# Kernel tuning notes

Hardware: AMD Instinct MI355X
Metric: run time of the kernel (lower is better)

## Reference

```python
import jax, jax.numpy as jnp
import numpy as np

NEG_SLOPE = 0.01  # torch nn.LeakyReLU default

N_NODES = 100000
N_EDGES = 1000000
D_FEAT = 64


def setup_inputs() -> dict:
    key = jax.random.key(0)
    ks = jax.random.split(key, 8)
    x = jax.random.normal(ks[0], (N_NODES, D_FEAT), dtype=jnp.float32)
    src = jax.random.randint(ks[1], (N_EDGES,), 0, N_NODES, dtype=jnp.int64 if jax.config.jax_enable_x64 else jnp.int32)
    dst = jax.random.randint(ks[2], (N_EDGES,), 0, N_NODES, dtype=jnp.int64 if jax.config.jax_enable_x64 else jnp.int32)
    s = 1.0 / np.sqrt(D_FEAT)
    W1 = jax.random.normal(ks[3], (D_FEAT, 64), dtype=jnp.float32) * s
    b1 = jnp.zeros((64,), dtype=jnp.float32)
    W2 = jax.random.normal(ks[4], (64, 64), dtype=jnp.float32) * s
    b2 = jnp.zeros((64,), dtype=jnp.float32)
    Wc = jax.random.normal(ks[5], (64, 2), dtype=jnp.float32) * s
    bc = jnp.zeros((2,), dtype=jnp.float32)
    return {"x": x, "src": src, "dst": dst, "W1": W1, "b1": b1,
            "W2": W2, "b2": b2, "Wc": Wc, "bc": bc}


def _graph_conv(x, src, dst, W, b, out_deg_isqrt, in_deg_isqrt, n_nodes):
    # DGL GraphConv, norm='both': h_v = ( sum_{u->v} x_u / sqrt(d_out(u)) ) / sqrt(d_in(v)) @ W + b
    # (in_feats <= out_feats here, so aggregate first then transform, matching DGL order)
    h = x * out_deg_isqrt[:, None]          # [N, d] scale by source out-degree
    msg = h[src]                            # [E, d] gather
    agg = jax.ops.segment_sum(msg, dst, num_segments=n_nodes)  # [N, d] scatter-add
    agg = agg * in_deg_isqrt[:, None]
    return agg @ W + b


def reference(x, src, dst, W1, b1, W2, b2, Wc, bc):
    n = x.shape[0]
    ones_e = jnp.ones(src.shape[0], dtype=x.dtype)
    out_deg = jnp.clip(jax.ops.segment_sum(ones_e, src, num_segments=n), 1.0)
    in_deg = jnp.clip(jax.ops.segment_sum(ones_e, dst, num_segments=n), 1.0)
    out_isqrt = out_deg ** -0.5
    in_isqrt = in_deg ** -0.5

    h = _graph_conv(x, src, dst, W1, b1, out_isqrt, in_isqrt, n)
    h = jax.nn.leaky_relu(h, NEG_SLOPE)
    h = _graph_conv(h, src, dst, W2, b2, out_isqrt, in_isqrt, n)
    h = jax.nn.leaky_relu(h, NEG_SLOPE)
    return h @ Wc + bc  # prediction=True -> linear classifier
```

## Files before the change

### kernel.cpp

```cpp
#include <hip/hip_runtime.h>


typedef __attribute__((ext_vector_type(8))) short short8;
typedef __attribute__((ext_vector_type(4))) float f32x4;

#define NPB 256
#define BSH 9
#define BW  512

__device__ __forceinline__ float b2f(unsigned short u) {
    return __uint_as_float(((unsigned int)u) << 16);
}
__device__ __forceinline__ unsigned short f2b(float f) {
    unsigned int i = __float_as_uint(f);
    unsigned int r = (i + 0x7FFFu + ((i >> 16) & 1u)) >> 16;
    return (unsigned short)r;
}

__global__ __launch_bounds__(256) void count_kernel(
    const int* __restrict__ src, const int* __restrict__ dst,
    int* __restrict__ cntD, int* __restrict__ cntS, int e, int chunk) {
    __shared__ int hD[256], hS[256];
    int t = threadIdx.x, pb = blockIdx.x;
    hD[t] = 0; hS[t] = 0;
    __syncthreads();
    int e0 = pb * chunk, e1 = min(e, e0 + chunk);
    for (int i = e0 + t; i < e1; i += 256) {
        atomicAdd(&hD[dst[i] >> BSH], 1);
        atomicAdd(&hS[src[i] >> BSH], 1);
    }
    __syncthreads();
    cntD[t * NPB + pb] = hD[t];
    cntS[t * NPB + pb] = hS[t];
}

__global__ __launch_bounds__(1024) void scanmat_kernel(int* __restrict__ cntD,
                                                       int* __restrict__ cntS) {
    int* a = (blockIdx.x == 0) ? cntD : cntS;
    __shared__ int s[1024];
    int t = threadIdx.x;
    int base = t * 64;
    int sum = 0;
    for (int j = 0; j < 64; j++) sum += a[base + j];
    s[t] = sum;
    __syncthreads();
    for (int d = 1; d < 1024; d <<= 1) {
        int x = (t >= d) ? s[t - d] : 0;
        __syncthreads();
        s[t] += x;
        __syncthreads();
    }
    int run = s[t] - sum;
    for (int j = 0; j < 64; j++) {
        int v = a[base + j];
        a[base + j] = run;
        run += v;
    }
}

__global__ __launch_bounds__(256) void part_kernel(
    const int* __restrict__ src, const int* __restrict__ dst,
    const int* __restrict__ cntD, const int* __restrict__ cntS,
    unsigned int* __restrict__ ebuf, unsigned short* __restrict__ sbuf,
    int e, int chunk) {
    __shared__ int cD[256], cS[256];
    int t = threadIdx.x, pb = blockIdx.x;
    cD[t] = cntD[t * NPB + pb];
    cS[t] = cntS[t * NPB + pb];
    __syncthreads();
    int e0 = pb * chunk, e1 = min(e, e0 + chunk);
    for (int i = e0 + t; i < e1; i += 256) {
        int s_ = src[i], d_ = dst[i];
        int pd = atomicAdd(&cD[d_ >> BSH], 1);
        ebuf[pd] = ((unsigned int)s_ << BSH) | (unsigned int)(d_ & (BW - 1));
        int ps_ = atomicAdd(&cS[s_ >> BSH], 1);
        sbuf[ps_] = (unsigned short)(s_ & (BW - 1));
    }
}

__global__ __launch_bounds__(256) void bucket_kernel(
    const unsigned int* __restrict__ ebuf, const unsigned short* __restrict__ sbuf,
    const int* __restrict__ cntD, const int* __restrict__ cntS,
    const float4* __restrict__ x4,
    int* __restrict__ row, float* __restrict__ ii, float* __restrict__ oi,
    int* __restrict__ csr, ushort4* __restrict__ xb, int n, int e) {
    __shared__ int cnt[BW], cur[BW], ocnt[BW], ps[256];
    __shared__ float ol[BW];
    int t = threadIdx.x, b = blockIdx.x;
    int v0 = b << BSH;
    int eb0 = cntD[b * NPB], eb1 = cntD[(b + 1) * NPB];
    int sb0 = cntS[b * NPB], sb1 = cntS[(b + 1) * NPB];
    cnt[t] = 0; cnt[t + 256] = 0;
    ocnt[t] = 0; ocnt[t + 256] = 0;
    __syncthreads();
    for (int i = eb0 + t; i < eb1; i += 256)
        atomicAdd(&cnt[ebuf[i] & (BW - 1)], 1);
    for (int i = sb0 + t; i < sb1; i += 256)
        atomicAdd(&ocnt[sbuf[i]], 1);
    __syncthreads();
    int c0 = cnt[2 * t], c1 = cnt[2 * t + 1];
    int pair = c0 + c1;
    ps[t] = pair;
    __syncthreads();
    for (int d = 1; d < 256; d <<= 1) {
        int x = (t >= d) ? ps[t - d] : 0;
        __syncthreads();
        ps[t] += x;
        __syncthreads();
    }
    int excl = ps[t] - pair;
    cur[2 * t] = excl;
    cur[2 * t + 1] = excl + c0;
    int v = v0 + 2 * t;
    if (v < n) {
        row[v] = eb0 + excl;
        ii[v] = rsqrtf((float)max(c0, 1));
    }
    if (v + 1 < n) {
        row[v + 1] = eb0 + excl + c0;
        ii[v + 1] = rsqrtf((float)max(c1, 1));
    }
    if (b == 0 && t == 0) row[n] = e;
    for (int j = t; j < BW; j += 256) {
        float o = rsqrtf((float)max(ocnt[j], 1));
        ol[j] = o;
        int vv = v0 + j;
        if (vv < n) oi[vv] = o;
    }
    __syncthreads();
    for (int i = eb0 + t; i < eb1; i += 256) {
        unsigned int p = ebuf[i];
        int r = atomicAdd(&cur[p & (BW - 1)], 1);
        csr[eb0 + r] = (int)(p >> BSH);
    }
    int nloc = min(BW, n - v0);
    for (int i = t; i < nloc * 16; i += 256) {
        int vl = i >> 4, q = i & 15;
        float s = ol[vl];
        float4 val = x4[(size_t)(v0 + vl) * 16 + q];
        xb[(size_t)(v0 + vl) * 16 + q] =
            make_ushort4(f2b(val.x * s), f2b(val.y * s), f2b(val.z * s), f2b(val.w * s));
    }
}

__global__ __launch_bounds__(256) void agg_kernel(
    const short8* __restrict__ featb, const int* __restrict__ row,
    const int* __restrict__ csr, const float* __restrict__ ii,
    short8* __restrict__ outb, int n, int nwaves) {
    int lane = threadIdx.x & 63;
    int o = lane >> 3, s = lane & 7;
    int wid = blockIdx.x * (blockDim.x >> 6) + (threadIdx.x >> 6);
    int ngroups = (n + 7) >> 3;

    for (int g = wid; g < ngroups; g += nwaves) {
        int v = (g << 3) + o;
        bool valid = v < n;
        int base = 0, cnt = 0;
        if (valid) { base = row[v]; cnt = row[v + 1] - base; }
        float a[8];
#pragma unroll
        for (int k = 0; k < 8; k++) a[k] = 0.f;
        int j = 0;
        for (; j + 3 < cnt; j += 4) {
            int u[4];
#pragma unroll
            for (int k = 0; k < 4; k++) u[k] = csr[base + j + k];
#pragma unroll
            for (int k = 0; k < 4; k++) {
                short8 f = featb[(size_t)u[k] * 8 + s];
#pragma unroll
                for (int m = 0; m < 8; m++)
                    a[m] += b2f((unsigned short)f[m]);
            }
        }
        for (; j < cnt; j++) {
            short8 f = featb[(size_t)csr[base + j] * 8 + s];
#pragma unroll
            for (int m = 0; m < 8; m++)
                a[m] += b2f((unsigned short)f[m]);
        }
        if (valid) {
            float iiv = ii[v];
            short8 r;
#pragma unroll
            for (int m = 0; m < 8; m++) r[m] = (short)f2b(a[m] * iiv);
            outb[(size_t)v * 8 + s] = r;
        }
    }
}

template <bool FINAL>
__global__ __launch_bounds__(256) void gemm_kernel(
    const unsigned short* __restrict__ aggb,
    const float* __restrict__ oi,
    const float* __restrict__ W, const float* __restrict__ bias,
    const float* __restrict__ Wc, const float* __restrict__ bcl,
    void* __restrict__ out, int n, int nwaves) {
    int lane = threadIdx.x & 63;
    int m15 = lane & 15, quad = lane >> 4;
    int wid = blockIdx.x * (blockDim.x >> 6) + (threadIdx.x >> 6);
    int ngroups = (n + 15) >> 4;

    short8 bf[4][2];
#pragma unroll
    for (int nt = 0; nt < 4; nt++)
#pragma unroll
        for (int kk = 0; kk < 2; kk++)
#pragma unroll
            for (int j = 0; j < 8; j++)
                bf[nt][kk][j] = (short)f2b(W[(kk * 32 + quad * 8 + j) * 64 + nt * 16 + m15]);

    float bias_r[4];
#pragma unroll
    for (int nt = 0; nt < 4; nt++) bias_r[nt] = bias[nt * 16 + m15];

    float wc_r[4][2];
    float bc0 = 0.f, bc1 = 0.f;
    if constexpr (FINAL) {
#pragma unroll
        for (int nt = 0; nt < 4; nt++) {
            wc_r[nt][0] = Wc[(nt * 16 + m15) * 2];
            wc_r[nt][1] = Wc[(nt * 16 + m15) * 2 + 1];
        }
        bc0 = bcl[0];
        bc1 = bcl[1];
    }

    for (int g = wid; g < ngroups; g += nwaves) {
        int rbase = g << 4;
        int rm = min(rbase + m15, n - 1);

        const short8* arow = (const short8*)(aggb + (size_t)rm * 64);
        short8 af0 = arow[quad];
        short8 af1 = arow[4 + quad];

        f32x4 acc[4];
#pragma unroll
        for (int nt = 0; nt < 4; nt++) {
            f32x4 z = {0.f, 0.f, 0.f, 0.f};
            z = __builtin_amdgcn_mfma_f32_16x16x32_bf16(af0, bf[nt][0], z, 0, 0, 0);
            z = __builtin_amdgcn_mfma_f32_16x16x32_bf16(af1, bf[nt][1], z, 0, 0, 0);
            acc[nt] = z;
        }

        if constexpr (!FINAL) {
#pragma unroll
            for (int r = 0; r < 4; r++) {
                int vr = rbase + quad * 4 + r;
                float os = (vr < n) ? oi[vr] : 0.f;
#pragma unroll
                for (int nt = 0; nt < 4; nt++) {
                    float o = acc[nt][r] + bias_r[nt];
                    o = (o > 0.f) ? o : 0.01f * o;
                    if (vr < n)
                        ((unsigned short*)out)[(size_t)vr * 64 + nt * 16 + m15] = f2b(o * os);
                }
            }
        } else {
#pragma unroll
            for (int r = 0; r < 4; r++) {
                float p0 = 0.f, p1 = 0.f;
#pragma unroll
                for (int nt = 0; nt < 4; nt++) {
                    float o = acc[nt][r] + bias_r[nt];
                    o = (o > 0.f) ? o : 0.01f * o;
                    p0 = fmaf(o, wc_r[nt][0], p0);
                    p1 = fmaf(o, wc_r[nt][1], p1);
                }
#pragma unroll
                for (int off = 1; off < 16; off <<= 1) {
                    p0 += __shfl_xor(p0, off);
                    p1 += __shfl_xor(p1, off);
                }
                int vr = rbase + quad * 4 + r;
                if (m15 == 0 && vr < n)
                    ((float2*)out)[vr] = make_float2(p0 + bc0, p1 + bc1);
            }
        }
    }
}

extern "C" void kernel_launch(void* const* d_in, const int* in_sizes, int n_in,
                              void* d_out, int out_size, void* d_ws, size_t ws_size,
                              hipStream_t stream) {
    const float* x  = (const float*)d_in[0];
    const int* src  = (const int*)d_in[1];
    const int* dst  = (const int*)d_in[2];
    const float* W1 = (const float*)d_in[3];
    const float* b1 = (const float*)d_in[4];
    const float* W2 = (const float*)d_in[5];
    const float* b2 = (const float*)d_in[6];
    const float* Wc = (const float*)d_in[7];
    const float* bc = (const float*)d_in[8];
    int n = in_sizes[0] / 64;
    int e = in_sizes[1];
    int total = n * 64;
    int nbuck = (n + BW - 1) >> BSH;

    char* ws = (char*)d_ws;
    size_t off = 0;
    auto take = [&](size_t bytes) -> char* {
        char* p = ws + off;
        off = (off + bytes + 255) & ~(size_t)255;
        return p;
    };
    int* cntD = (int*)take(256 * NPB * 4);
    int* cntS = (int*)take(256 * NPB * 4);
    unsigned int* ebuf = (unsigned int*)take((size_t)e * 4);
    unsigned short* sbuf = (unsigned short*)take((size_t)e * 2);
    int* row  = (int*)take((size_t)(n + 1) * 4);
    int* csr  = (int*)take((size_t)e * 4);
    float* oi = (float*)take((size_t)n * 4);
    float* ii = (float*)take((size_t)n * 4);
    unsigned short* xb  = (unsigned short*)take((size_t)total * 2);
    unsigned short* h1b = (unsigned short*)take((size_t)total * 2);
    unsigned short* aggb = (unsigned short*)take((size_t)total * 2);

    const int tb = 256;
    int chunk = (e + NPB - 1) / NPB;

    count_kernel<<<NPB, tb, 0, stream>>>(src, dst, cntD, cntS, e, chunk);
    scanmat_kernel<<<2, 1024, 0, stream>>>(cntD, cntS);
    part_kernel<<<NPB, tb, 0, stream>>>(src, dst, cntD, cntS, ebuf, sbuf, e, chunk);
    bucket_kernel<<<nbuck, tb, 0, stream>>>(ebuf, sbuf, cntD, cntS, (const float4*)x,
                                            row, ii, oi, csr, (ushort4*)xb, n, e);

    const int ablocks = 2048;
    const int awaves = ablocks * (tb / 64);
    const int gblocks = 512;
    const int gwaves = gblocks * (tb / 64);

    agg_kernel<<<ablocks, tb, 0, stream>>>((const short8*)xb, row, csr, ii,
                                           (short8*)aggb, n, awaves);
    gemm_kernel<false><<<gblocks, tb, 0, stream>>>(aggb, oi, W1, b1,
                                                   nullptr, nullptr, h1b, n, gwaves);
    agg_kernel<<<ablocks, tb, 0, stream>>>((const short8*)h1b, row, csr, ii,
                                           (short8*)aggb, n, awaves);
    gemm_kernel<true><<<gblocks, tb, 0, stream>>>(aggb, oi, W2, b2,
                                                  Wc, bc, d_out, n, gwaves);
}
```

Measured before the change: 221.7 us.

## Fuse neighbor aggregation with MFMA transform via per-wave LDS tile

Merges the gather-aggregate kernel and the dense transform kernel into one: each wave aggregates 16 destination nodes into a padded shared-memory tile, then feeds it straight to the bf16 MFMA and epilogue. This removes the intermediate aggregate buffer write/read and two kernel launches per layer. In exchange, the grid shrinks from 2048 aggregation blocks to 784, so fewer waves are available to hide gather latency. Each wave also now serializes two aggregation passes before its matrix op.

Measured after the change: 221.8 us. No clear change (+0.0%).

```diff
diff --git a/kernel.cpp b/kernel.cpp
--- a/kernel.cpp
+++ b/kernel.cpp
@@ -143,61 +143,19 @@
     }
 }
 
-__global__ __launch_bounds__(256) void agg_kernel(
+template <bool FINAL>
+__global__ __launch_bounds__(256) void fused_kernel(
     const short8* __restrict__ featb, const int* __restrict__ row,
     const int* __restrict__ csr, const float* __restrict__ ii,
-    short8* __restrict__ outb, int n, int nwaves) {
-    int lane = threadIdx.x & 63;
-    int o = lane >> 3, s = lane & 7;
-    int wid = blockIdx.x * (blockDim.x >> 6) + (threadIdx.x >> 6);
-    int ngroups = (n + 7) >> 3;
-
-    for (int g = wid; g < ngroups; g += nwaves) {
-        int v = (g << 3) + o;
-        bool valid = v < n;
-        int base = 0, cnt = 0;
-        if (valid) { base = row[v]; cnt = row[v + 1] - base; }
-        float a[8];
-#pragma unroll
-        for (int k = 0; k < 8; k++) a[k] = 0.f;
-        int j = 0;
-        for (; j + 3 < cnt; j += 4) {
-            int u[4];
-#pragma unroll
-            for (int k = 0; k < 4; k++) u[k] = csr[base + j + k];
-#pragma unroll
-            for (int k = 0; k < 4; k++) {
-                short8 f = featb[(size_t)u[k] * 8 + s];
-#pragma unroll
-                for (int m = 0; m < 8; m++)
-                    a[m] += b2f((unsigned short)f[m]);
-            }
-        }
-        for (; j < cnt; j++) {
-            short8 f = featb[(size_t)csr[base + j] * 8 + s];
-#pragma unroll
-            for (int m = 0; m < 8; m++)
-                a[m] += b2f((unsigned short)f[m]);
-        }
-        if (valid) {
-            float iiv = ii[v];
-            short8 r;
-#pragma unroll
-            for (int m = 0; m < 8; m++) r[m] = (short)f2b(a[m] * iiv);
-            outb[(size_t)v * 8 + s] = r;
-        }
-    }
-}
-
-template <bool FINAL>
-__global__ __launch_bounds__(256) void gemm_kernel(
-    const unsigned short* __restrict__ aggb,
     const float* __restrict__ oi,
     const float* __restrict__ W, const float* __restrict__ bias,
     const float* __restrict__ Wc, const float* __restrict__ bcl,
     void* __restrict__ out, int n, int nwaves) {
+    __shared__ short8 tile[4][16 * 9];
     int lane = threadIdx.x & 63;
+    int o = lane >> 3, s = lane & 7;
     int m15 = lane & 15, quad = lane >> 4;
+    short8* tl = tile[threadIdx.x >> 6];
     int wid = blockIdx.x * (blockDim.x >> 6) + (threadIdx.x >> 6);
     int ngroups = (n + 15) >> 4;
 
@@ -228,11 +186,44 @@
 
     for (int g = wid; g < ngroups; g += nwaves) {
         int rbase = g << 4;
-        int rm = min(rbase + m15, n - 1);
-
-        const short8* arow = (const short8*)(aggb + (size_t)rm * 64);
-        short8 af0 = arow[quad];
-        short8 af1 = arow[4 + quad];
+
+#pragma unroll
+        for (int p = 0; p < 2; p++) {
+            int v = rbase + p * 8 + o;
+            bool valid = v < n;
+            int base = 0, cnt = 0;
+            if (valid) { base = row[v]; cnt = row[v + 1] - base; }
+            float a[8];
+#pragma unroll
+            for (int k = 0; k < 8; k++) a[k] = 0.f;
+            int j = 0;
+            for (; j + 3 < cnt; j += 4) {
+                int u[4];
+#pragma unroll
+                for (int k = 0; k < 4; k++) u[k] = csr[base + j + k];
+#pragma unroll
+                for (int k = 0; k < 4; k++) {
+                    short8 f = featb[(size_t)u[k] * 8 + s];
+#pragma unroll
+                    for (int m = 0; m < 8; m++)
+                        a[m] += b2f((unsigned short)f[m]);
+                }
+            }
+            for (; j < cnt; j++) {
+                short8 f = featb[(size_t)csr[base + j] * 8 + s];
+#pragma unroll
+                for (int m = 0; m < 8; m++)
+                    a[m] += b2f((unsigned short)f[m]);
+            }
+            float iiv = valid ? ii[v] : 0.f;
+            short8 r;
+#pragma unroll
+            for (int m = 0; m < 8; m++) r[m] = (short)f2b(a[m] * iiv);
+            tl[(p * 8 + o) * 9 + s] = r;
+        }
+
+        short8 af0 = tl[m15 * 9 + quad];
+        short8 af1 = tl[m15 * 9 + 4 + quad];
 
         f32x4 acc[4];
 #pragma unroll
@@ -250,10 +241,10 @@
                 float os = (vr < n) ? oi[vr] : 0.f;
 #pragma unroll
                 for (int nt = 0; nt < 4; nt++) {
-                    float o = acc[nt][r] + bias_r[nt];
-                    o = (o > 0.f) ? o : 0.01f * o;
+                    float ov = acc[nt][r] + bias_r[nt];
+                    ov = (ov > 0.f) ? ov : 0.01f * ov;
                     if (vr < n)
-                        ((unsigned short*)out)[(size_t)vr * 64 + nt * 16 + m15] = f2b(o * os);
+                        ((unsigned short*)out)[(size_t)vr * 64 + nt * 16 + m15] = f2b(ov * os);
                 }
             }
         } else {
@@ -262,10 +253,10 @@
                 float p0 = 0.f, p1 = 0.f;
 #pragma unroll
                 for (int nt = 0; nt < 4; nt++) {
-                    float o = acc[nt][r] + bias_r[nt];
-                    o = (o > 0.f) ? o : 0.01f * o;
-                    p0 = fmaf(o, wc_r[nt][0], p0);
-                    p1 = fmaf(o, wc_r[nt][1], p1);
+                    float ov = acc[nt][r] + bias_r[nt];
+                    ov = (ov > 0.f) ? ov : 0.01f * ov;
+                    p0 = fmaf(ov, wc_r[nt][0], p0);
+                    p1 = fmaf(ov, wc_r[nt][1], p1);
                 }
 #pragma unroll
                 for (int off = 1; off < 16; off <<= 1) {
@@ -314,7 +305,6 @@
     float* ii = (float*)take((size_t)n * 4);
     unsigned short* xb  = (unsigned short*)take((size_t)total * 2);
     unsigned short* h1b = (unsigned short*)take((size_t)total * 2);
-    unsigned short* aggb = (unsigned short*)take((size_t)total * 2);
 
     const int tb = 256;
     int chunk = (e + NPB - 1) / NPB;
@@ -325,17 +315,11 @@
     bucket_kernel<<<nbuck, tb, 0, stream>>>(ebuf, sbuf, cntD, cntS, (const float4*)x,
                                             row, ii, oi, csr, (ushort4*)xb, n, e);
 
-    const int ablocks = 2048;
-    const int awaves = ablocks * (tb / 64);
-    const int gblocks = 512;
-    const int gwaves = gblocks * (tb / 64);
-
-    agg_kernel<<<ablocks, tb, 0, stream>>>((const short8*)xb, row, csr, ii,
-                                           (short8*)aggb, n, awaves);
-    gemm_kernel<false><<<gblocks, tb, 0, stream>>>(aggb, oi, W1, b1,
-                                                   nullptr, nullptr, h1b, n, gwaves);
-    agg_kernel<<<ablocks, tb, 0, stream>>>((const short8*)h1b, row, csr, ii,
-                                           (short8*)aggb, n, awaves);
-    gemm_kernel<true><<<gblocks, tb, 0, stream>>>(aggb, oi, W2, b2,
-                                                  Wc, bc, d_out, n, gwaves);
-}
+    const int fblocks = 784;
+    const int fwaves = fblocks * (tb / 64);
+
+    fused_kernel<false><<<fblocks, tb, 0, stream>>>((const short8*)xb, row, csr, ii, oi,
+                                                    W1, b1, nullptr, nullptr, h1b, n, fwaves);
+    fused_kernel<true><<<fblocks, tb, 0, stream>>>((const short8*)h1b, row, csr, ii, nullptr,
+                                                   W2, b2, Wc, bc, d_out, n, fwaves);
+}
```
